# Optimization experiments

Hardware: AMD Instinct MI355X
Metric: run time of the kernel (lower is better)

The kernel has to match this reference:

```python
import jax, jax.numpy as jnp
import numpy as np

DIM = 2048       # model dim
HID = 1024       # expert hidden dim
E = 8            # num_experts
K = 2            # top_k
SHID = HID * 1   # shared expert hidden = hidden_dim * num_shared_experts
INIT = 0.02


def setup_inputs() -> dict:
    key = jax.random.key(0)
    ks = jax.random.split(key, 9)
    return {
        "x": jax.random.normal(ks[0], (2, 1024, DIM), jnp.float32),
        "expert_bias": jnp.zeros((E,), jnp.float32),
        "gate_w": jax.random.normal(ks[1], (E, DIM), jnp.float32) * INIT,
        "w1": jax.random.normal(ks[2], (E, HID, DIM), jnp.float32) * INIT,
        "w2": jax.random.normal(ks[3], (E, DIM, HID), jnp.float32) * INIT,
        "w3": jax.random.normal(ks[4], (E, HID, DIM), jnp.float32) * INIT,
        "sw1": jax.random.normal(ks[5], (SHID, DIM), jnp.float32) * INIT,
        "sw2": jax.random.normal(ks[6], (DIM, SHID), jnp.float32) * INIT,
        "sw3": jax.random.normal(ks[7], (SHID, DIM), jnp.float32) * INIT,
    }


def reference(x, expert_bias, gate_w, w1, w2, w3, sw1, sw2, sw3):
    B, S, D = x.shape
    xf = x.reshape(-1, D)                      # [N, D]
    N = xf.shape[0]

    # --- TokenChoiceTopKRouter (sigmoid score, bias-adjusted top-k selection) ---
    scores = jax.nn.sigmoid((xf @ gate_w.T).astype(jnp.float32))      # [N, E]
    _, sel = jax.lax.top_k(scores + expert_bias[None, :], K)          # [N, K] indices
    top_scores = jnp.take_along_axis(scores, sel, axis=1)             # [N, K] (route_norm=False, route_scale=1.0)

    # --- TokenReorderer: stable sort routed slots by expert id ---
    flat_exp = sel.reshape(-1)                                        # [N*K]
    order = jnp.argsort(flat_exp, stable=True)                        # expert-sorted slot order
    sorted_exp = flat_exp[order]                                      # [N*K]
    tok_idx = order // K                                              # source token per slot
    sc_sorted = top_scores.reshape(-1)[order]                         # [N*K]

    # score_before_experts=True: scale input by routing score before expert FFN
    rin = xf[tok_idx] * sc_sorted[:, None].astype(x.dtype)            # [N*K, D]

    # --- GroupedExperts: per-expert SwiGLU on the expert-sorted token block ---
    # (grouped GEMM expressed as a masked loop over the fixed expert set)
    out_sorted = jnp.zeros_like(rin)
    for e in range(E):
        m = (sorted_exp == e)[:, None].astype(rin.dtype)
        h = jax.nn.silu(rin @ w1[e].T) * (rin @ w3[e].T)              # [N*K, HID]
        out_sorted = out_sorted + m * (h @ w2[e].T)

    # combine: scatter-add expert outputs back to tokens
    routed = jnp.zeros((N, D), x.dtype).at[tok_idx].add(out_sorted)

    # shared expert (plain SwiGLU FeedForward)
    shared = (jax.nn.silu(xf @ sw1.T) * (xf @ sw3.T)) @ sw2.T

    return (routed + shared).reshape(B, S, D)
```

## Files before the change

### kernel.cpp

```cpp
#include <hip/hip_runtime.h>
#include <hip/hip_bf16.h>
#include <stdint.h>

#define DIMM 2048
#define HIDD 1024
#define NEXP 8
#define TOPK 2
#define NTOK 2048
#define CAP_E 1024
#define SH_BASE (NEXP * CAP_E)
#define NROW (SH_BASE + NTOK)

typedef __bf16 bf16_t;
typedef __bf16 bf16x4 __attribute__((ext_vector_type(4)));
typedef __bf16 bf16x8 __attribute__((ext_vector_type(8)));
typedef float f32x4 __attribute__((ext_vector_type(4)));

__device__ __forceinline__ void gl2lds16(const bf16_t* g, bf16_t* l) {
    __builtin_amdgcn_global_load_lds(
        (const __attribute__((address_space(1))) void*)g,
        (__attribute__((address_space(3))) void*)l, 16, 0, 0);
}

__global__ __launch_bounds__(256) void zero_f(float* __restrict__ p, int n4) {
    int i = blockIdx.x * 256 + threadIdx.x;
    if (i < n4) ((float4*)p)[i] = (float4){0.f, 0.f, 0.f, 0.f};
}

__global__ __launch_bounds__(256) void router_k(const float* __restrict__ x,
                                                const float* __restrict__ gw,
                                                const float* __restrict__ bias,
                                                int* __restrict__ sel,
                                                float* __restrict__ topsc) {
    int t = blockIdx.x;
    int tid = threadIdx.x;
    const float* xr = x + (long)t * DIMM;
    double acc[NEXP];
#pragma unroll
    for (int e = 0; e < NEXP; ++e) acc[e] = 0.0;
    for (int d = tid; d < DIMM; d += 256) {
        double xv = (double)xr[d];
#pragma unroll
        for (int e = 0; e < NEXP; ++e) acc[e] += xv * (double)gw[e * DIMM + d];
    }
#pragma unroll
    for (int off = 32; off >= 1; off >>= 1)
#pragma unroll
        for (int e = 0; e < NEXP; ++e) acc[e] += __shfl_down(acc[e], off, 64);
    __shared__ double red[4][NEXP];
    int lane = tid & 63, w = tid >> 6;
    if (lane == 0)
#pragma unroll
        for (int e = 0; e < NEXP; ++e) red[w][e] = acc[e];
    __syncthreads();
    if (tid == 0) {
        double sc[NEXP], v[NEXP];
#pragma unroll
        for (int e = 0; e < NEXP; ++e) {
            double s = red[0][e] + red[1][e] + red[2][e] + red[3][e];
            sc[e] = 1.0 / (1.0 + exp(-s));
            v[e] = sc[e] + (double)bias[e];
        }
        int b0 = 0;
        for (int e = 1; e < NEXP; ++e) if (v[e] > v[b0]) b0 = e;
        int b1 = -1;
        for (int e = 0; e < NEXP; ++e)
            if (e != b0 && (b1 < 0 || v[e] > v[b1])) b1 = e;
        sel[t * 2] = b0; sel[t * 2 + 1] = b1;
        topsc[t * 2] = (float)sc[b0]; topsc[t * 2 + 1] = (float)sc[b1];
    }
}

__global__ __launch_bounds__(256) void sort_k(const int* __restrict__ sel,
                                              const float* __restrict__ topsc,
                                              int* __restrict__ tok_s,
                                              float* __restrict__ sc_s,
                                              int* __restrict__ counts) {
    __shared__ int se[NTOK * TOPK];
    int tid = threadIdx.x;
    for (int i = tid; i < NTOK * TOPK; i += 256) se[i] = sel[i];
    __syncthreads();
    int wv = tid >> 6, lane = tid & 63;
    unsigned long long lower = (1ull << lane) - 1ull;
    for (int ei = 0; ei < 2; ++ei) {
        int e = wv * 2 + ei;
        int base = e * CAP_E;
        int off = 0;
        for (int c = 0; c < (NTOK * TOPK) / 64; ++c) {
            int slot = c * 64 + lane;
            bool m = (se[slot] == e);
            unsigned long long bal = __ballot(m);
            if (m) {
                int rank = off + __popcll(bal & lower);
                if (rank < CAP_E) {
                    tok_s[base + rank] = slot >> 1;
                    sc_s[base + rank] = topsc[slot];
                }
            }
            off += __popcll(bal);
        }
        int cnt = min(off, CAP_E);
        if (lane == 0) counts[e] = cnt;
        int padded = min((cnt + 127) & ~127, CAP_E);
        for (int r = cnt + lane; r < padded; r += 64) tok_s[base + r] = -1;
    }
}

__global__ __launch_bounds__(256) void build_rin(const float* __restrict__ x,
                                                 const int* __restrict__ tok_s,
                                                 const float* __restrict__ sc_s,
                                                 const int* __restrict__ counts,
                                                 bf16_t* __restrict__ rin) {
    int row = blockIdx.x;
    int tok; float sc = 1.0f;
    if (row >= SH_BASE) {
        tok = row - SH_BASE;
    } else {
        int e = row >> 10, r = row & (CAP_E - 1);
        int cnt = min(counts[e], CAP_E);
        int padded = min((cnt + 127) & ~127, CAP_E);
        if (r >= padded) return;
        if (r < cnt) { tok = tok_s[row]; sc = sc_s[row]; }
        else tok = -1;
    }
    int d0 = threadIdx.x * 8;
    bf16x8 o;
    if (tok >= 0) {
        const float* src = x + (long)tok * DIMM + d0;
        float4 a = *(const float4*)src;
        float4 b = *(const float4*)(src + 4);
        o[0] = (bf16_t)(a.x * sc); o[1] = (bf16_t)(a.y * sc);
        o[2] = (bf16_t)(a.z * sc); o[3] = (bf16_t)(a.w * sc);
        o[4] = (bf16_t)(b.x * sc); o[5] = (bf16_t)(b.y * sc);
        o[6] = (bf16_t)(b.z * sc); o[7] = (bf16_t)(b.w * sc);
    } else {
#pragma unroll
        for (int i = 0; i < 8; ++i) o[i] = (bf16_t)0.0f;
    }
    *(bf16x8*)(rin + (long)row * DIMM + d0) = o;
}

template <int PHASE>
__global__ __launch_bounds__(256, 2) void gemm_moe(
    const bf16_t* __restrict__ A0,
    const float* __restrict__ W1, const float* __restrict__ W3,
    const float* __restrict__ SW1, const float* __restrict__ SW3,
    bf16_t* __restrict__ Cout, float* __restrict__ outp,
    const int* __restrict__ counts, const int* __restrict__ tok_s) {
    constexpr int K = (PHASE == 1) ? 2048 : 1024;
    int g = blockIdx.z;
    int base = (g < 8) ? g * CAP_E : SH_BASE;
    int M = NTOK;
    if (g < 8) {
        int c = min(counts[g], CAP_E);
        M = min((c + 127) & ~127, CAP_E);
    }
    int m0 = blockIdx.y * 128;
    if (m0 >= M) return;
    int n0 = blockIdx.x * 128;
    const bf16_t* A = A0 + (long)base * K;

    __shared__ bf16_t lA[128 * 64];
    __shared__ bf16_t lB[128 * 64];

    int tid = threadIdx.x;
    int lane = tid & 63, wv = tid >> 6;
    int quad = lane >> 4, l16 = lane & 15;
    int wm = (wv & 1) * 64, wn = (wv >> 1) * 64;
    int cc = tid & 7;
    int rbase = tid >> 3;

    const float* brow[4];
    int slot[4];
#pragma unroll
    for (int i = 0; i < 4; ++i) {
        int row = i * 32 + rbase;
        int n = n0 + row;
        const float* p;
        if (PHASE == 1) {
            if (g < 8) p = (n < HIDD) ? W1 + ((long)g << 21) + (long)n * DIMM
                                      : W3 + ((long)g << 21) + (long)(n - HIDD) * DIMM;
            else       p = (n < HIDD) ? SW1 + (long)n * DIMM
                                      : SW3 + (long)(n - HIDD) * DIMM;
        } else {
            p = (g < 8) ? W1 + ((long)g << 21) + (long)n * HIDD
                        : SW1 + (long)n * HIDD;
        }
        brow[i] = p + cc * 8;
        slot[i] = row * 8 + (cc ^ (row & 7));
    }

    f32x4 acc[4][4];
#pragma unroll
    for (int i = 0; i < 4; ++i)
#pragma unroll
        for (int j = 0; j < 4; ++j) acc[i][j] = (f32x4){0.f, 0.f, 0.f, 0.f};

    for (int kt = 0; kt < K / 64; ++kt) {
        int kb = kt * 64;
#pragma unroll
        for (int i = 0; i < 4; ++i) {
            int row = i * 32 + rbase;
            int scc = cc ^ (row & 7);
            gl2lds16(A + (long)(m0 + row) * K + kb + scc * 8, &lA[(i * 256 + tid) * 8]);
        }
        float4 u[4], v[4];
#pragma unroll
        for (int i = 0; i < 4; ++i) {
            const float* p = brow[i] + kb;
            u[i] = *(const float4*)p;
            v[i] = *(const float4*)(p + 4);
        }
#pragma unroll
        for (int i = 0; i < 4; ++i) {
            bf16x8 o = {(bf16_t)u[i].x, (bf16_t)u[i].y, (bf16_t)u[i].z, (bf16_t)u[i].w,
                        (bf16_t)v[i].x, (bf16_t)v[i].y, (bf16_t)v[i].z, (bf16_t)v[i].w};
            *(bf16x8*)&lB[slot[i] * 8] = o;
        }
        __syncthreads();
#pragma unroll
        for (int ki = 0; ki < 2; ++ki) {
            bf16x8 af[4], bfr[4];
            int kc = ki * 4 + quad;
#pragma unroll
            for (int mi = 0; mi < 4; ++mi) {
                int row = wm + mi * 16 + l16;
                int chunk = row * 8 + (kc ^ (row & 7));
                af[mi] = *(const bf16x8*)&lA[chunk * 8];
            }
#pragma unroll
            for (int ni = 0; ni < 4; ++ni) {
                int row = wn + ni * 16 + l16;
                int chunk = row * 8 + (kc ^ (row & 7));
                bfr[ni] = *(const bf16x8*)&lB[chunk * 8];
            }
#pragma unroll
            for (int mi = 0; mi < 4; ++mi)
#pragma unroll
                for (int ni = 0; ni < 4; ++ni)
                    acc[mi][ni] = __builtin_amdgcn_mfma_f32_16x16x32_bf16(
                        af[mi], bfr[ni], acc[mi][ni], 0, 0, 0);
        }
        __syncthreads();
    }

    if (PHASE == 1) {
#pragma unroll
        for (int mi = 0; mi < 4; ++mi)
#pragma unroll
            for (int r = 0; r < 4; ++r) {
                int row = base + m0 + wm + mi * 16 + quad * 4 + r;
#pragma unroll
                for (int ni = 0; ni < 4; ++ni) {
                    int col = n0 + wn + ni * 16 + l16;
                    Cout[(long)row * DIMM + col] = (bf16_t)acc[mi][ni][r];
                }
            }
    } else {
#pragma unroll
        for (int mi = 0; mi < 4; ++mi)
#pragma unroll
            for (int r = 0; r < 4; ++r) {
                int rloc = m0 + wm + mi * 16 + quad * 4 + r;
                int tok = (g < 8) ? tok_s[g * CAP_E + rloc] : rloc;
                if (tok >= 0) {
                    float* op = outp + (long)tok * DIMM + n0 + wn + l16;
#pragma unroll
                    for (int ni = 0; ni < 4; ++ni)
                        atomicAdd(op + ni * 16, acc[mi][ni][r]);
                }
            }
    }
}

__global__ __launch_bounds__(256) void silu_comb(const bf16_t* __restrict__ ht,
                                                 bf16_t* __restrict__ h,
                                                 const int* __restrict__ counts) {
    int row = blockIdx.x;
    if (row < SH_BASE) {
        int e = row >> 10, r = row & (CAP_E - 1);
        int cnt = min(counts[e], CAP_E);
        int padded = min((cnt + 127) & ~127, CAP_E);
        if (r >= padded) return;
    }
    int j = threadIdx.x * 4;
    bf16x4 a4 = *(const bf16x4*)&ht[(long)row * DIMM + j];
    bf16x4 b4 = *(const bf16x4*)&ht[(long)row * DIMM + HIDD + j];
    bf16x4 o;
#pragma unroll
    for (int i = 0; i < 4; ++i) {
        float a = (float)a4[i], b = (float)b4[i];
        float s = a / (1.f + expf(-a));
        o[i] = (bf16_t)(s * b);
    }
    *(bf16x4*)&h[(long)row * HIDD + j] = o;
}

extern "C" void kernel_launch(void* const* d_in, const int* in_sizes, int n_in,
                              void* d_out, int out_size, void* d_ws, size_t ws_size,
                              hipStream_t stream) {
    const float* x    = (const float*)d_in[0];
    const float* bias = (const float*)d_in[1];
    const float* gw   = (const float*)d_in[2];
    const float* w1   = (const float*)d_in[3];
    const float* w2   = (const float*)d_in[4];
    const float* w3   = (const float*)d_in[5];
    const float* sw1  = (const float*)d_in[6];
    const float* sw2  = (const float*)d_in[7];
    const float* sw3  = (const float*)d_in[8];
    float* out = (float*)d_out;

    char* p = (char*)d_ws;
    auto alloc = [&](size_t bytes) {
        char* r = p;
        p += (bytes + 255) & ~(size_t)255;
        return r;
    };
    bf16_t* rin   = (bf16_t*)alloc((size_t)NROW * DIMM * 2);
    bf16_t* ht    = (bf16_t*)alloc((size_t)NROW * DIMM * 2);
    bf16_t* hB    = (bf16_t*)alloc((size_t)NROW * HIDD * 2);
    int*   sel    = (int*)alloc(NTOK * TOPK * 4);
    float* topsc  = (float*)alloc(NTOK * TOPK * 4);
    int*   tok_s  = (int*)alloc(SH_BASE * 4);
    float* sc_s   = (float*)alloc(SH_BASE * 4);
    int*   counts = (int*)alloc(256);

    zero_f<<<(NTOK * DIMM / 4) / 256, 256, 0, stream>>>(out, NTOK * DIMM / 4);
    router_k<<<NTOK, 256, 0, stream>>>(x, gw, bias, sel, topsc);
    sort_k<<<1, 256, 0, stream>>>(sel, topsc, tok_s, sc_s, counts);
    build_rin<<<NROW, 256, 0, stream>>>(x, tok_s, sc_s, counts, rin);

    gemm_moe<1><<<dim3(16, 16, 9), 256, 0, stream>>>(
        rin, w1, w3, sw1, sw3, ht, nullptr, counts, nullptr);

    silu_comb<<<NROW, 256, 0, stream>>>(ht, hB, counts);

    gemm_moe<2><<<dim3(16, 16, 9), 256, 0, stream>>>(
        hB, w2, nullptr, sw2, nullptr, nullptr, out, counts, tok_s);
}
```

Baseline: 479.4 us.

## Double-buffer MoE GEMMs, fuse SwiGLU into first GEMM, replace atomics with gather combine

```diff
diff --git a/kernel.cpp b/kernel.cpp
--- a/kernel.cpp
+++ b/kernel.cpp
@@ -20,11 +20,6 @@
     __builtin_amdgcn_global_load_lds(
         (const __attribute__((address_space(1))) void*)g,
         (__attribute__((address_space(3))) void*)l, 16, 0, 0);
-}
-
-__global__ __launch_bounds__(256) void zero_f(float* __restrict__ p, int n4) {
-    int i = blockIdx.x * 256 + threadIdx.x;
-    if (i < n4) ((float4*)p)[i] = (float4){0.f, 0.f, 0.f, 0.f};
 }
 
 __global__ __launch_bounds__(256) void router_k(const float* __restrict__ x,
@@ -75,7 +70,8 @@
                                               const float* __restrict__ topsc,
                                               int* __restrict__ tok_s,
                                               float* __restrict__ sc_s,
-                                              int* __restrict__ counts) {
+                                              int* __restrict__ counts,
+                                              int* __restrict__ pos) {
     __shared__ int se[NTOK * TOPK];
     int tid = threadIdx.x;
     for (int i = tid; i < NTOK * TOPK; i += 256) se[i] = sel[i];
@@ -95,6 +91,9 @@
                 if (rank < CAP_E) {
                     tok_s[base + rank] = slot >> 1;
                     sc_s[base + rank] = topsc[slot];
+                    pos[slot] = base + rank;
+                } else {
+                    pos[slot] = -1;
                 }
             }
             off += __popcll(bal);
@@ -140,14 +139,66 @@
     *(bf16x8*)(rin + (long)row * DIMM + d0) = o;
 }
 
+
+#define STAGE_A(kt, buf) do { \
+    _Pragma("unroll") \
+    for (int i_ = 0; i_ < 4; ++i_) \
+        gl2lds16(arow[i_] + (kt) * 64, &lA[buf][(i_ * 256 + tid) * 8]); \
+} while (0)
+
+#define LOAD_B(kt, s) do { \
+    _Pragma("unroll") \
+    for (int i_ = 0; i_ < 4; ++i_) { \
+        const float* bp_ = brow[i_] + (kt) * 64; \
+        u##s[i_] = *(const float4*)bp_; \
+        v##s[i_] = *(const float4*)(bp_ + 4); \
+    } \
+} while (0)
+
+#define WRITE_B(s, buf) do { \
+    _Pragma("unroll") \
+    for (int i_ = 0; i_ < 4; ++i_) { \
+        bf16x8 o_ = {(bf16_t)u##s[i_].x, (bf16_t)u##s[i_].y, \
+                     (bf16_t)u##s[i_].z, (bf16_t)u##s[i_].w, \
+                     (bf16_t)v##s[i_].x, (bf16_t)v##s[i_].y, \
+                     (bf16_t)v##s[i_].z, (bf16_t)v##s[i_].w}; \
+        *(bf16x8*)&lB[buf][slot[i_] * 8] = o_; \
+    } \
+} while (0)
+
+#define MFMA_TILE(buf) do { \
+    _Pragma("unroll") \
+    for (int ki_ = 0; ki_ < 2; ++ki_) { \
+        bf16x8 af_[4], bg_[4]; \
+        int kc_ = ki_ * 4 + quad; \
+        _Pragma("unroll") \
+        for (int mi_ = 0; mi_ < 4; ++mi_) { \
+            int row_ = wm + mi_ * 16 + l16; \
+            af_[mi_] = *(const bf16x8*)&lA[buf][(row_ * 8 + (kc_ ^ (row_ & 7))) * 8]; \
+        } \
+        _Pragma("unroll") \
+        for (int ni_ = 0; ni_ < 4; ++ni_) { \
+            int row_ = wn + ni_ * 16 + l16; \
+            bg_[ni_] = *(const bf16x8*)&lB[buf][(row_ * 8 + (kc_ ^ (row_ & 7))) * 8]; \
+        } \
+        _Pragma("unroll") \
+        for (int mi_ = 0; mi_ < 4; ++mi_) \
+            _Pragma("unroll") \
+            for (int ni_ = 0; ni_ < 4; ++ni_) \
+                acc[mi_][ni_] = __builtin_amdgcn_mfma_f32_16x16x32_bf16( \
+                    af_[mi_], bg_[ni_], acc[mi_][ni_], 0, 0, 0); \
+    } \
+} while (0)
+
 template <int PHASE>
 __global__ __launch_bounds__(256, 2) void gemm_moe(
     const bf16_t* __restrict__ A0,
     const float* __restrict__ W1, const float* __restrict__ W3,
     const float* __restrict__ SW1, const float* __restrict__ SW3,
-    bf16_t* __restrict__ Cout, float* __restrict__ outp,
-    const int* __restrict__ counts, const int* __restrict__ tok_s) {
+    bf16_t* __restrict__ hOut, float* __restrict__ C2,
+    const int* __restrict__ counts) {
     constexpr int K = (PHASE == 1) ? 2048 : 1024;
+    constexpr int KT = K / 64;
     int g = blockIdx.z;
     int base = (g < 8) ? g * CAP_E : SH_BASE;
     int M = NTOK;
@@ -157,11 +208,10 @@
     }
     int m0 = blockIdx.y * 128;
     if (m0 >= M) return;
-    int n0 = blockIdx.x * 128;
     const bf16_t* A = A0 + (long)base * K;
 
-    __shared__ bf16_t lA[128 * 64];
-    __shared__ bf16_t lB[128 * 64];
+    __shared__ bf16_t lA[2][128 * 64];
+    __shared__ bf16_t lB[2][128 * 64];
 
     int tid = threadIdx.x;
     int lane = tid & 63, wv = tid >> 6;
@@ -170,24 +220,29 @@
     int cc = tid & 7;
     int rbase = tid >> 3;
 
+    const bf16_t* arow[4];
+#pragma unroll
+    for (int i = 0; i < 4; ++i) {
+        int row = i * 32 + rbase;
+        arow[i] = A + (long)(m0 + row) * K + (cc ^ (row & 7)) * 8;
+    }
     const float* brow[4];
     int slot[4];
 #pragma unroll
     for (int i = 0; i < 4; ++i) {
-        int row = i * 32 + rbase;
-        int n = n0 + row;
+        int r = i * 32 + rbase;
         const float* p;
         if (PHASE == 1) {
-            if (g < 8) p = (n < HIDD) ? W1 + ((long)g << 21) + (long)n * DIMM
-                                      : W3 + ((long)g << 21) + (long)(n - HIDD) * DIMM;
-            else       p = (n < HIDD) ? SW1 + (long)n * DIMM
-                                      : SW3 + (long)(n - HIDD) * DIMM;
+            int colw = (blockIdx.x << 6) + ((r >> 5) << 4) + (r & 15);
+            int type = (r >> 4) & 1;
+            if (g < 8) p = (type ? W3 : W1) + ((long)g << 21) + (long)colw * DIMM;
+            else       p = (type ? SW3 : SW1) + (long)colw * DIMM;
         } else {
-            p = (g < 8) ? W1 + ((long)g << 21) + (long)n * HIDD
-                        : SW1 + (long)n * HIDD;
+            int n = (blockIdx.x << 7) + r;
+            p = ((g < 8) ? W1 + ((long)g << 21) : SW1) + (long)n * HIDD;
         }
         brow[i] = p + cc * 8;
-        slot[i] = row * 8 + (cc ^ (row & 7));
+        slot[i] = r * 8 + (cc ^ (r & 7));
     }
 
     f32x4 acc[4][4];
@@ -196,52 +251,26 @@
 #pragma unroll
         for (int j = 0; j < 4; ++j) acc[i][j] = (f32x4){0.f, 0.f, 0.f, 0.f};
 
-    for (int kt = 0; kt < K / 64; ++kt) {
-        int kb = kt * 64;
-#pragma unroll
-        for (int i = 0; i < 4; ++i) {
-            int row = i * 32 + rbase;
-            int scc = cc ^ (row & 7);
-            gl2lds16(A + (long)(m0 + row) * K + kb + scc * 8, &lA[(i * 256 + tid) * 8]);
+    float4 u0[4], v0[4], u1[4], v1[4];
+    STAGE_A(0, 0);
+    LOAD_B(0, 0);
+    WRITE_B(0, 0);
+    LOAD_B(1, 1);
+    __syncthreads();
+
+    for (int kt = 0; kt < KT; kt += 2) {
+        STAGE_A(kt + 1, 1);
+        if (kt + 2 < KT) LOAD_B(kt + 2, 0);
+        MFMA_TILE(0);
+        WRITE_B(1, 1);
+        __syncthreads();
+        if (kt + 2 < KT) {
+            STAGE_A(kt + 2, 0);
+            if (kt + 3 < KT) LOAD_B(kt + 3, 1);
         }
-        float4 u[4], v[4];
-#pragma unroll
-        for (int i = 0; i < 4; ++i) {
-            const float* p = brow[i] + kb;
-            u[i] = *(const float4*)p;
-            v[i] = *(const float4*)(p + 4);
-        }
-#pragma unroll
-        for (int i = 0; i < 4; ++i) {
-            bf16x8 o = {(bf16_t)u[i].x, (bf16_t)u[i].y, (bf16_t)u[i].z, (bf16_t)u[i].w,
-                        (bf16_t)v[i].x, (bf16_t)v[i].y, (bf16_t)v[i].z, (bf16_t)v[i].w};
-            *(bf16x8*)&lB[slot[i] * 8] = o;
-        }
+        MFMA_TILE(1);
+        if (kt + 2 < KT) WRITE_B(0, 0);
         __syncthreads();
-#pragma unroll
-        for (int ki = 0; ki < 2; ++ki) {
-            bf16x8 af[4], bfr[4];
-            int kc = ki * 4 + quad;
-#pragma unroll
-            for (int mi = 0; mi < 4; ++mi) {
-                int row = wm + mi * 16 + l16;
-                int chunk = row * 8 + (kc ^ (row & 7));
-                af[mi] = *(const bf16x8*)&lA[chunk * 8];
-            }
-#pragma unroll
-            for (int ni = 0; ni < 4; ++ni) {
-                int row = wn + ni * 16 + l16;
-                int chunk = row * 8 + (kc ^ (row & 7));
-                bfr[ni] = *(const bf16x8*)&lB[chunk * 8];
-            }
-#pragma unroll
-            for (int mi = 0; mi < 4; ++mi)
-#pragma unroll
-                for (int ni = 0; ni < 4; ++ni)
-                    acc[mi][ni] = __builtin_amdgcn_mfma_f32_16x16x32_bf16(
-                        af[mi], bfr[ni], acc[mi][ni], 0, 0, 0);
-        }
-        __syncthreads();
     }
 
     if (PHASE == 1) {
@@ -249,11 +278,14 @@
         for (int mi = 0; mi < 4; ++mi)
 #pragma unroll
             for (int r = 0; r < 4; ++r) {
-                int row = base + m0 + wm + mi * 16 + quad * 4 + r;
-#pragma unroll
-                for (int ni = 0; ni < 4; ++ni) {
-                    int col = n0 + wn + ni * 16 + l16;
-                    Cout[(long)row * DIMM + col] = (bf16_t)acc[mi][ni][r];
+                long row = base + m0 + wm + mi * 16 + quad * 4 + r;
+#pragma unroll
+                for (int j = 0; j < 2; ++j) {
+                    float gt = acc[mi][2 * j][r];
+                    float up = acc[mi][2 * j + 1][r];
+                    float s = gt / (1.f + __expf(-gt));
+                    int col = (blockIdx.x << 6) + ((wn >> 5) + j) * 16 + l16;
+                    hOut[row * HIDD + col] = (bf16_t)(s * up);
                 }
             }
     } else {
@@ -261,39 +293,40 @@
         for (int mi = 0; mi < 4; ++mi)
 #pragma unroll
             for (int r = 0; r < 4; ++r) {
-                int rloc = m0 + wm + mi * 16 + quad * 4 + r;
-                int tok = (g < 8) ? tok_s[g * CAP_E + rloc] : rloc;
-                if (tok >= 0) {
-                    float* op = outp + (long)tok * DIMM + n0 + wn + l16;
-#pragma unroll
-                    for (int ni = 0; ni < 4; ++ni)
-                        atomicAdd(op + ni * 16, acc[mi][ni][r]);
+                long row = base + m0 + wm + mi * 16 + quad * 4 + r;
+#pragma unroll
+                for (int ni = 0; ni < 4; ++ni) {
+                    int col = (blockIdx.x << 7) + wn + ni * 16 + l16;
+                    C2[row * DIMM + col] = acc[mi][ni][r];
                 }
             }
     }
 }
 
-__global__ __launch_bounds__(256) void silu_comb(const bf16_t* __restrict__ ht,
-                                                 bf16_t* __restrict__ h,
-                                                 const int* __restrict__ counts) {
-    int row = blockIdx.x;
-    if (row < SH_BASE) {
-        int e = row >> 10, r = row & (CAP_E - 1);
-        int cnt = min(counts[e], CAP_E);
-        int padded = min((cnt + 127) & ~127, CAP_E);
-        if (r >= padded) return;
-    }
-    int j = threadIdx.x * 4;
-    bf16x4 a4 = *(const bf16x4*)&ht[(long)row * DIMM + j];
-    bf16x4 b4 = *(const bf16x4*)&ht[(long)row * DIMM + HIDD + j];
-    bf16x4 o;
-#pragma unroll
-    for (int i = 0; i < 4; ++i) {
-        float a = (float)a4[i], b = (float)b4[i];
-        float s = a / (1.f + expf(-a));
-        o[i] = (bf16_t)(s * b);
-    }
-    *(bf16x4*)&h[(long)row * HIDD + j] = o;
+__global__ __launch_bounds__(256) void combine_k(const float* __restrict__ C2,
+                                                 const int* __restrict__ pos,
+                                                 float* __restrict__ out) {
+    int t = blockIdx.x;
+    int c = threadIdx.x * 8;
+    int p0 = pos[t * 2], p1 = pos[t * 2 + 1];
+    const float* sh = C2 + (long)(SH_BASE + t) * DIMM + c;
+    float4 a = *(const float4*)sh;
+    float4 b = *(const float4*)(sh + 4);
+    if (p0 >= 0) {
+        const float* q = C2 + (long)p0 * DIMM + c;
+        float4 qa = *(const float4*)q, qb = *(const float4*)(q + 4);
+        a.x += qa.x; a.y += qa.y; a.z += qa.z; a.w += qa.w;
+        b.x += qb.x; b.y += qb.y; b.z += qb.z; b.w += qb.w;
+    }
+    if (p1 >= 0) {
+        const float* q = C2 + (long)p1 * DIMM + c;
+        float4 qa = *(const float4*)q, qb = *(const float4*)(q + 4);
+        a.x += qa.x; a.y += qa.y; a.z += qa.z; a.w += qa.w;
+        b.x += qb.x; b.y += qb.y; b.z += qb.z; b.w += qb.w;
+    }
+    float* op = out + (long)t * DIMM + c;
+    *(float4*)op = a;
+    *(float4*)(op + 4) = b;
 }
 
 extern "C" void kernel_launch(void* const* d_in, const int* in_sizes, int n_in,
@@ -317,24 +350,24 @@
         return r;
     };
     bf16_t* rin   = (bf16_t*)alloc((size_t)NROW * DIMM * 2);
-    bf16_t* ht    = (bf16_t*)alloc((size_t)NROW * DIMM * 2);
     bf16_t* hB    = (bf16_t*)alloc((size_t)NROW * HIDD * 2);
+    float*  C2    = (float*)alloc((size_t)NROW * DIMM * 4);
     int*   sel    = (int*)alloc(NTOK * TOPK * 4);
     float* topsc  = (float*)alloc(NTOK * TOPK * 4);
     int*   tok_s  = (int*)alloc(SH_BASE * 4);
     float* sc_s   = (float*)alloc(SH_BASE * 4);
+    int*   pos    = (int*)alloc(NTOK * TOPK * 4);
     int*   counts = (int*)alloc(256);
 
-    zero_f<<<(NTOK * DIMM / 4) / 256, 256, 0, stream>>>(out, NTOK * DIMM / 4);
     router_k<<<NTOK, 256, 0, stream>>>(x, gw, bias, sel, topsc);
-    sort_k<<<1, 256, 0, stream>>>(sel, topsc, tok_s, sc_s, counts);
+    sort_k<<<1, 256, 0, stream>>>(sel, topsc, tok_s, sc_s, counts, pos);
     build_rin<<<NROW, 256, 0, stream>>>(x, tok_s, sc_s, counts, rin);
 
     gemm_moe<1><<<dim3(16, 16, 9), 256, 0, stream>>>(
-        rin, w1, w3, sw1, sw3, ht, nullptr, counts, nullptr);
-
-    silu_comb<<<NROW, 256, 0, stream>>>(ht, hB, counts);
+        rin, w1, w3, sw1, sw3, hB, nullptr, counts);
 
     gemm_moe<2><<<dim3(16, 16, 9), 256, 0, stream>>>(
-        hB, w2, nullptr, sw2, nullptr, nullptr, out, counts, tok_s);
-}
+        hB, w2, nullptr, sw2, nullptr, nullptr, C2, counts);
+
+    combine_k<<<NTOK, 256, 0, stream>>>(C2, pos, out);
+}
```

After: 416.2 us. 1.15x faster.
